# Optimization experiments

Measured on AMD Instinct MI355X. Metric: run time of the kernel, lower is better.

## Reference

```python
import jax, jax.numpy as jnp
import numpy as np

N_NODES = 100000
N_EDGES = 3200000
EMB_DIM = 128


def setup_inputs() -> dict:
    key = jax.random.key(0)
    k_emb, k_w1, k_w2, k_e = jax.random.split(key, 4)
    emb = jax.random.normal(k_emb, (N_NODES, EMB_DIM), dtype=jnp.float32)
    W1 = jax.random.normal(k_w1, (EMB_DIM, 64), dtype=jnp.float32) * (1.0 / np.sqrt(EMB_DIM))
    b1 = jnp.zeros((64,), dtype=jnp.float32)
    W2 = jax.random.normal(k_w2, (64, 32), dtype=jnp.float32) * (1.0 / np.sqrt(64))
    b2 = jnp.zeros((32,), dtype=jnp.float32)
    edge_index = jax.random.randint(k_e, (2, N_EDGES), 0, N_NODES, dtype=jnp.int64)
    return {"embedding": emb, "W1": W1, "b1": b1, "W2": W2, "b2": b2,
            "edge_index": edge_index}


def gcn_conv(x, W, b, src, dst, n):
    # PyG GCNConv defaults: add self-loops, symmetric normalization D^-1/2 (A+I) D^-1/2,
    # linear transform first, then gather-scale-scatter aggregation, then bias.
    xw = x @ W                                                  # [N, out]
    ones = jnp.ones(src.shape, dtype=xw.dtype)
    deg = jax.ops.segment_sum(ones, dst, num_segments=n) + 1.0  # in-degree + self-loop
    dis = jax.lax.rsqrt(deg)                                    # deg >= 1 always
    norm = dis[src] * dis[dst]                                  # [E]
    agg = jax.ops.segment_sum(xw[src] * norm[:, None], dst, num_segments=n)
    agg = agg + (dis * dis)[:, None] * xw                       # self-loop messages
    return agg + b


def reference(embedding, W1, b1, W2, b2, edge_index):
    n = embedding.shape[0]
    src, dst = edge_index[0], edge_index[1]
    # encode
    h = jax.nn.relu(gcn_conv(embedding, W1, b1, src, dst, n))
    z = gcn_conv(h, W2, b2, src, dst, n)                        # [N, 32]
    # decode: per-edge gather-dot-sigmoid
    logits = jnp.sum(z[src] * z[dst], axis=1)                   # [E]
    return jax.nn.sigmoid(logits)
```

## Files before the change

kernel.cpp:

```cpp
#include <hip/hip_runtime.h>
#include <hip/hip_bf16.h>
#include <math.h>

#define NN 100000
#define NE 3200000
#define NPAD 100096
#define NB 196
#define BN 512
#define EPB 8192
#define NBLK 391

__device__ __forceinline__ unsigned short bf16_of(float x) {
    __hip_bfloat16 h = __float2bfloat16(x);
    return *(unsigned short*)&h;
}
__device__ __forceinline__ unsigned pack2(float a, float b) {
    return (unsigned)bf16_of(a) | ((unsigned)bf16_of(b) << 16);
}
__device__ __forceinline__ float lo_f(unsigned u) { return __uint_as_float(u << 16); }
__device__ __forceinline__ float hi_f(unsigned u) { return __uint_as_float(u & 0xffff0000u); }
__device__ __forceinline__ void acc8(float* a, uint4 r) {
    a[0] += lo_f(r.x); a[1] += hi_f(r.x);
    a[2] += lo_f(r.y); a[3] += hi_f(r.y);
    a[4] += lo_f(r.z); a[5] += hi_f(r.z);
    a[6] += lo_f(r.w); a[7] += hi_f(r.w);
}

__global__ __launch_bounds__(256) void hist_kernel(const int* __restrict__ dst,
                                                   int* __restrict__ blkhist) {
    __shared__ int cnt[NB];
    int t = threadIdx.x;
    for (int i = t; i < NB; i += 256) cnt[i] = 0;
    __syncthreads();
    int e0 = blockIdx.x * EPB;
    int e1 = min(e0 + EPB, NE);
    for (int e = e0 + t; e < e1; e += 256) atomicAdd(&cnt[dst[e] >> 9], 1);
    __syncthreads();
    for (int i = t; i < NB; i += 256) blkhist[i * NBLK + blockIdx.x] = cnt[i];
}

__global__ __launch_bounds__(64) void scanA_kernel(int* __restrict__ blkhist,
                                                   int* __restrict__ totals) {
    int j = blockIdx.x, lane = threadIdx.x;
    int base = j * NBLK;
    int carry = 0;
    for (int c = 0; c < NBLK; c += 64) {
        int b = c + lane;
        int v = (b < NBLK) ? blkhist[base + b] : 0;
        int inc = v;
#pragma unroll
        for (int m = 1; m < 64; m <<= 1) {
            int u = __shfl_up(inc, m, 64);
            if (lane >= m) inc += u;
        }
        if (b < NBLK) blkhist[base + b] = carry + inc - v;
        carry += __shfl(inc, 63, 64);
    }
    if (lane == 0) totals[j] = carry;
}

__global__ __launch_bounds__(256) void scanB_kernel(const int* __restrict__ totals,
                                                    int* __restrict__ bucket_base) {
    __shared__ int sm[NB];
    int t = threadIdx.x;
    if (t < NB) sm[t] = totals[t];
    __syncthreads();
    if (t == 0) {
        int r = 0;
        for (int i = 0; i < NB; ++i) { bucket_base[i] = r; r += sm[i]; }
        bucket_base[NB] = r;
    }
}

__global__ __launch_bounds__(256) void scatter_kernel(const int* __restrict__ src,
                                                      const int* __restrict__ dst,
                                                      const int* __restrict__ blkhist,
                                                      const int* __restrict__ bucket_base,
                                                      int* __restrict__ staged) {
    __shared__ int cnt[NB];
    __shared__ int lbase[NB + 1];
    __shared__ int gbase[NB];
    __shared__ int sbuf[EPB];
    int t = threadIdx.x;
    for (int i = t; i < NB; i += 256) cnt[i] = 0;
    __syncthreads();
    int e0 = blockIdx.x * EPB;
    int e1 = min(e0 + EPB, NE);
    int cn = e1 - e0;
    for (int e = e0 + t; e < e1; e += 256) atomicAdd(&cnt[dst[e] >> 9], 1);
    __syncthreads();
    if (t < 64) {
        int v[4]; int s = 0;
#pragma unroll
        for (int k = 0; k < 4; ++k) { int idx = t * 4 + k; v[k] = (idx < NB) ? cnt[idx] : 0; s += v[k]; }
        int inc = s;
#pragma unroll
        for (int m = 1; m < 64; m <<= 1) {
            int u = __shfl_up(inc, m, 64);
            if (t >= m) inc += u;
        }
        int run = inc - s;
#pragma unroll
        for (int k = 0; k < 4; ++k) { int idx = t * 4 + k; if (idx < NB) lbase[idx] = run; run += v[k]; }
        if (t == 63) lbase[NB] = inc;
    }
    __syncthreads();
    for (int i = t; i < NB; i += 256) {
        gbase[i] = bucket_base[i] + blkhist[i * NBLK + blockIdx.x];
        cnt[i] = lbase[i];
    }
    __syncthreads();
    for (int e = e0 + t; e < e1; e += 256) {
        int s = src[e], d = dst[e];
        int r = atomicAdd(&cnt[d >> 9], 1);
        sbuf[r] = (s << 9) | (d & (BN - 1));
    }
    __syncthreads();
    for (int i = t; i < cn; i += 256) {
        int lo = 0, hi = NB - 1;
        while (lo < hi) { int mid = (lo + hi + 1) >> 1; if (lbase[mid] <= i) lo = mid; else hi = mid - 1; }
        staged[gbase[lo] + i - lbase[lo]] = sbuf[i];
    }
}

__global__ __launch_bounds__(256) void fine_kernel(const int* __restrict__ staged,
                                                   const int* __restrict__ bucket_base,
                                                   int* __restrict__ offset,
                                                   float* __restrict__ dis,
                                                   int* __restrict__ csr_src) {
    __shared__ int hist[BN];
    __shared__ int offs[BN];
    __shared__ int cur[BN];
    int t = threadIdx.x, j = blockIdx.x;
    int bb = bucket_base[j], be = bucket_base[j + 1];
    for (int i = t; i < BN; i += 256) hist[i] = 0;
    __syncthreads();
    for (int e = bb + t; e < be; e += 256) atomicAdd(&hist[staged[e] & (BN - 1)], 1);
    __syncthreads();
    if (t < 64) {
        int v[8]; int s = 0;
#pragma unroll
        for (int k = 0; k < 8; ++k) { v[k] = hist[t * 8 + k]; s += v[k]; }
        int inc = s;
#pragma unroll
        for (int m = 1; m < 64; m <<= 1) {
            int u = __shfl_up(inc, m, 64);
            if (t >= m) inc += u;
        }
        int run = inc - s;
#pragma unroll
        for (int k = 0; k < 8; ++k) { offs[t * 8 + k] = run; run += v[k]; }
    }
    __syncthreads();
    for (int l = t; l < BN; l += 256) {
        cur[l] = offs[l];
        int n = j * BN + l;
        if (n < NN) {
            offset[n] = bb + offs[l];
            dis[n] = rsqrtf((float)hist[l] + 1.0f);
        }
    }
    if (j == NB - 1 && t == 0) offset[NN] = NE;
    __syncthreads();
    for (int e = bb + t; e < be; e += 256) {
        int p = staged[e];
        int r = atomicAdd(&cur[p & (BN - 1)], 1);
        csr_src[bb + r] = p >> 9;
    }
}

__global__ __launch_bounds__(256) void mm1_kernel(const float* __restrict__ x,
                                                  const float* __restrict__ W,
                                                  const float* __restrict__ dis,
                                                  unsigned short* __restrict__ y) {
    __shared__ float Ws[128 * 64];
    __shared__ float xs[4][8][132];
    int t = threadIdx.x;
    for (int i = t; i < 128 * 64; i += 256) Ws[i] = W[i];
    int wave = t >> 6, lane = t & 63;
    int nsub = lane >> 3;
    int o8 = (lane & 7) * 8;
    int base = blockIdx.x * 32 + wave * 8;
#pragma unroll
    for (int r = 0; r < 8; ++r) {
        xs[wave][r][lane] = x[(size_t)(base + r) * 128 + lane];
        xs[wave][r][lane + 64] = x[(size_t)(base + r) * 128 + 64 + lane];
    }
    __syncthreads();
    float acc[8] = {0, 0, 0, 0, 0, 0, 0, 0};
#pragma unroll 16
    for (int k = 0; k < 128; ++k) {
        float a = xs[wave][nsub][k];
        const float4 w0 = *(const float4*)&Ws[k * 64 + o8];
        const float4 w1 = *(const float4*)&Ws[k * 64 + o8 + 4];
        acc[0] = fmaf(a, w0.x, acc[0]); acc[1] = fmaf(a, w0.y, acc[1]);
        acc[2] = fmaf(a, w0.z, acc[2]); acc[3] = fmaf(a, w0.w, acc[3]);
        acc[4] = fmaf(a, w1.x, acc[4]); acc[5] = fmaf(a, w1.y, acc[5]);
        acc[6] = fmaf(a, w1.z, acc[6]); acc[7] = fmaf(a, w1.w, acc[7]);
    }
    float sc = dis[base + nsub];
    uint4 o;
    o.x = pack2(acc[0] * sc, acc[1] * sc);
    o.y = pack2(acc[2] * sc, acc[3] * sc);
    o.z = pack2(acc[4] * sc, acc[5] * sc);
    o.w = pack2(acc[6] * sc, acc[7] * sc);
    *(uint4*)&y[(size_t)(base + nsub) * 64 + o8] = o;
}

__global__ __launch_bounds__(256) void mm2_kernel(const unsigned short* __restrict__ h,
                                                  const float* __restrict__ W,
                                                  const float* __restrict__ dis,
                                                  unsigned short* __restrict__ y) {
    __shared__ float Ws[64 * 32];
    __shared__ float hs[4][8][68];
    int t = threadIdx.x;
    for (int i = t; i < 64 * 32; i += 256) Ws[i] = W[i];
    int wave = t >> 6, lane = t & 63;
    int nsub = lane >> 3;
    int o4 = (lane & 7) * 4;
    int base = blockIdx.x * 32 + wave * 8;
    const unsigned* h2 = (const unsigned*)h;
#pragma unroll
    for (int rr = 0; rr < 4; ++rr) {
        int r = rr * 2 + (lane >> 5);
        unsigned u = h2[(size_t)(base + r) * 32 + (lane & 31)];
        hs[wave][r][(lane & 31) * 2] = lo_f(u);
        hs[wave][r][(lane & 31) * 2 + 1] = hi_f(u);
    }
    __syncthreads();
    float4 acc = {0.f, 0.f, 0.f, 0.f};
#pragma unroll 16
    for (int k = 0; k < 64; ++k) {
        float a = hs[wave][nsub][k];
        const float4 w = *(const float4*)&Ws[k * 32 + o4];
        acc.x = fmaf(a, w.x, acc.x);
        acc.y = fmaf(a, w.y, acc.y);
        acc.z = fmaf(a, w.z, acc.z);
        acc.w = fmaf(a, w.w, acc.w);
    }
    float sc = dis[base + nsub];
    ushort4 o;
    o.x = bf16_of(acc.x * sc); o.y = bf16_of(acc.y * sc);
    o.z = bf16_of(acc.z * sc); o.w = bf16_of(acc.w * sc);
    *(ushort4*)&y[(size_t)(base + nsub) * 32 + o4] = o;
}

__global__ __launch_bounds__(256) void agg64_kernel(const uint4* __restrict__ ys4,
                                                    const float* __restrict__ dis,
                                                    const int* __restrict__ offset,
                                                    const int* __restrict__ csr_src,
                                                    const float* __restrict__ b,
                                                    uint4* __restrict__ h4) {
    int tid = blockIdx.x * 256 + threadIdx.x;
    int nd = tid >> 3, c = tid & 7;
    if (nd >= NN) return;
    int start = offset[nd], end = offset[nd + 1];
    float acc[8] = {0, 0, 0, 0, 0, 0, 0, 0};
    acc8(acc, ys4[(size_t)nd * 8 + c]);
    int i = start;
    int n8 = start + ((end - start) & ~7);
    for (; i < n8; i += 8) {
        int s0 = csr_src[i],     s1 = csr_src[i + 1], s2 = csr_src[i + 2], s3 = csr_src[i + 3];
        int s4 = csr_src[i + 4], s5 = csr_src[i + 5], s6 = csr_src[i + 6], s7 = csr_src[i + 7];
        uint4 r0 = ys4[(size_t)s0 * 8 + c];
        uint4 r1 = ys4[(size_t)s1 * 8 + c];
        uint4 r2 = ys4[(size_t)s2 * 8 + c];
        uint4 r3 = ys4[(size_t)s3 * 8 + c];
        uint4 r4 = ys4[(size_t)s4 * 8 + c];
        uint4 r5 = ys4[(size_t)s5 * 8 + c];
        uint4 r6 = ys4[(size_t)s6 * 8 + c];
        uint4 r7 = ys4[(size_t)s7 * 8 + c];
        acc8(acc, r0); acc8(acc, r1); acc8(acc, r2); acc8(acc, r3);
        acc8(acc, r4); acc8(acc, r5); acc8(acc, r6); acc8(acc, r7);
    }
    for (; i < end; ++i) acc8(acc, ys4[(size_t)csr_src[i] * 8 + c]);
    float ds = dis[nd];
    const float4 bv0 = *(const float4*)&b[c * 8];
    const float4 bv1 = *(const float4*)&b[c * 8 + 4];
    uint4 o;
    o.x = pack2(fmaxf(fmaf(ds, acc[0], bv0.x), 0.f), fmaxf(fmaf(ds, acc[1], bv0.y), 0.f));
    o.y = pack2(fmaxf(fmaf(ds, acc[2], bv0.z), 0.f), fmaxf(fmaf(ds, acc[3], bv0.w), 0.f));
    o.z = pack2(fmaxf(fmaf(ds, acc[4], bv1.x), 0.f), fmaxf(fmaf(ds, acc[5], bv1.y), 0.f));
    o.w = pack2(fmaxf(fmaf(ds, acc[6], bv1.z), 0.f), fmaxf(fmaf(ds, acc[7], bv1.w), 0.f));
    h4[(size_t)nd * 8 + c] = o;
}

__global__ __launch_bounds__(256) void agg32_kernel(const uint4* __restrict__ ys4,
                                                    const float* __restrict__ dis,
                                                    const int* __restrict__ offset,
                                                    const int* __restrict__ csr_src,
                                                    const float* __restrict__ b,
                                                    uint4* __restrict__ z4) {
    int tid = blockIdx.x * 256 + threadIdx.x;
    int nd = tid >> 2, c = tid & 3;
    if (nd >= NN) return;
    int start = offset[nd], end = offset[nd + 1];
    float acc[8] = {0, 0, 0, 0, 0, 0, 0, 0};
    acc8(acc, ys4[(size_t)nd * 4 + c]);
    int i = start;
    int n8 = start + ((end - start) & ~7);
    for (; i < n8; i += 8) {
        int s0 = csr_src[i],     s1 = csr_src[i + 1], s2 = csr_src[i + 2], s3 = csr_src[i + 3];
        int s4 = csr_src[i + 4], s5 = csr_src[i + 5], s6 = csr_src[i + 6], s7 = csr_src[i + 7];
        uint4 r0 = ys4[(size_t)s0 * 4 + c];
        uint4 r1 = ys4[(size_t)s1 * 4 + c];
        uint4 r2 = ys4[(size_t)s2 * 4 + c];
        uint4 r3 = ys4[(size_t)s3 * 4 + c];
        uint4 r4 = ys4[(size_t)s4 * 4 + c];
        uint4 r5 = ys4[(size_t)s5 * 4 + c];
        uint4 r6 = ys4[(size_t)s6 * 4 + c];
        uint4 r7 = ys4[(size_t)s7 * 4 + c];
        acc8(acc, r0); acc8(acc, r1); acc8(acc, r2); acc8(acc, r3);
        acc8(acc, r4); acc8(acc, r5); acc8(acc, r6); acc8(acc, r7);
    }
    for (; i < end; ++i) acc8(acc, ys4[(size_t)csr_src[i] * 4 + c]);
    float ds = dis[nd];
    const float4 bv0 = *(const float4*)&b[c * 8];
    const float4 bv1 = *(const float4*)&b[c * 8 + 4];
    uint4 o;
    o.x = pack2(fmaf(ds, acc[0], bv0.x), fmaf(ds, acc[1], bv0.y));
    o.y = pack2(fmaf(ds, acc[2], bv0.z), fmaf(ds, acc[3], bv0.w));
    o.z = pack2(fmaf(ds, acc[4], bv1.x), fmaf(ds, acc[5], bv1.y));
    o.w = pack2(fmaf(ds, acc[6], bv1.z), fmaf(ds, acc[7], bv1.w));
    z4[(size_t)nd * 4 + c] = o;
}

__global__ __launch_bounds__(256) void decode_kernel(const uint4* __restrict__ z4,
                                                     const int* __restrict__ src,
                                                     const int* __restrict__ dst,
                                                     float* __restrict__ out) {
    int tid = blockIdx.x * 256 + threadIdx.x;
    int e = tid >> 2, k = tid & 3;
    if (e >= NE) return;
    int s = src[e], d = dst[e];
    uint4 ra = z4[(size_t)s * 4 + k];
    uint4 rb = z4[(size_t)d * 4 + k];
    float acc;
    acc  = lo_f(ra.x) * lo_f(rb.x) + hi_f(ra.x) * hi_f(rb.x);
    acc += lo_f(ra.y) * lo_f(rb.y) + hi_f(ra.y) * hi_f(rb.y);
    acc += lo_f(ra.z) * lo_f(rb.z) + hi_f(ra.z) * hi_f(rb.z);
    acc += lo_f(ra.w) * lo_f(rb.w) + hi_f(ra.w) * hi_f(rb.w);
#pragma unroll
    for (int m = 2; m >= 1; m >>= 1) acc += __shfl_xor(acc, m, 4);
    if (k == 0) out[e] = 1.0f / (1.0f + expf(-acc));
}

extern "C" void kernel_launch(void* const* d_in, const int* in_sizes, int n_in,
                              void* d_out, int out_size, void* d_ws, size_t ws_size,
                              hipStream_t stream) {
    const float* emb = (const float*)d_in[0];
    const float* W1  = (const float*)d_in[1];
    const float* b1  = (const float*)d_in[2];
    const float* W2  = (const float*)d_in[3];
    const float* b2  = (const float*)d_in[4];
    const int*   ei  = (const int*)d_in[5];
    const int* src = ei;
    const int* dst = ei + NE;
    float* out = (float*)d_out;

    char* w = (char*)d_ws;
    int*   offset      = (int*)w;           w += (size_t)NPAD * 4;
    float* dis         = (float*)w;         w += (size_t)NPAD * 4;
    int*   bucket_base = (int*)w;           w += 1024;
    int*   totals      = (int*)w;           w += 1024;
    int*   blkhist     = (int*)w;           w += 307200;
    int*   csr_src     = (int*)w;           w += (size_t)NE * 4;
    int*   staged      = (int*)w;           w += (size_t)NE * 4;
    unsigned short* ysbuf = (unsigned short*)w; w += (size_t)NN * 64 * 2;
    unsigned short* h  = (unsigned short*)w;
    unsigned short* ys1 = ysbuf;
    unsigned short* ys2 = ysbuf;
    unsigned short* z   = ysbuf + (size_t)NN * 32;

    hist_kernel<<<NBLK, 256, 0, stream>>>(dst, blkhist);
    scanA_kernel<<<NB, 64, 0, stream>>>(blkhist, totals);
    scanB_kernel<<<1, 256, 0, stream>>>(totals, bucket_base);
    scatter_kernel<<<NBLK, 256, 0, stream>>>(src, dst, blkhist, bucket_base, staged);
    fine_kernel<<<NB, 256, 0, stream>>>(staged, bucket_base, offset, dis, csr_src);

    mm1_kernel<<<NN / 32, 256, 0, stream>>>(emb, W1, dis, ys1);
    agg64_kernel<<<(NN * 8) / 256, 256, 0, stream>>>((const uint4*)ys1, dis, offset, csr_src, b1, (uint4*)h);

    mm2_kernel<<<NN / 32, 256, 0, stream>>>(h, W2, dis, ys2);
    agg32_kernel<<<(NN * 4 + 255) / 256, 256, 0, stream>>>((const uint4*)ys2, dis, offset, csr_src, b2, (uint4*)z);

    decode_kernel<<<(NE * 4) / 256, 256, 0, stream>>>((const uint4*)z, src, dst, out);
}
```

Baseline: 398.3 us.

## Use bf16 MFMA for both dense transforms and store bucket ids in scatter

Both node-feature matmuls (128→64 and 64→32) move from scalar FP32 FMA loops to bf16 16x16x32 MFMA instructions. The weights are held transposed in LDS and kept in registers, and each wave processes four 16-row tiles over a 391-block grid. mm1 now converts the FP32 embedding input to bf16 before the matmul, which lowers precision. Separately, the scatter kernel records each edge's bucket id in shared memory, replacing a per-element binary search during write-out at the cost of 8 KB more LDS.

After: 363.3 us. 8.8% less time.

```diff
diff --git a/kernel.cpp b/kernel.cpp
--- a/kernel.cpp
+++ b/kernel.cpp
@@ -9,6 +9,9 @@
 #define BN 512
 #define EPB 8192
 #define NBLK 391
+
+typedef __attribute__((ext_vector_type(8))) short short8;
+typedef __attribute__((ext_vector_type(4))) float floatx4;
 
 __device__ __forceinline__ unsigned short bf16_of(float x) {
     __hip_bfloat16 h = __float2bfloat16(x);
@@ -81,6 +84,7 @@
     __shared__ int lbase[NB + 1];
     __shared__ int gbase[NB];
     __shared__ int sbuf[EPB];
+    __shared__ unsigned char sbkt[EPB];
     int t = threadIdx.x;
     for (int i = t; i < NB; i += 256) cnt[i] = 0;
     __syncthreads();
@@ -112,14 +116,15 @@
     __syncthreads();
     for (int e = e0 + t; e < e1; e += 256) {
         int s = src[e], d = dst[e];
-        int r = atomicAdd(&cnt[d >> 9], 1);
+        int bk = d >> 9;
+        int r = atomicAdd(&cnt[bk], 1);
         sbuf[r] = (s << 9) | (d & (BN - 1));
+        sbkt[r] = (unsigned char)bk;
     }
     __syncthreads();
     for (int i = t; i < cn; i += 256) {
-        int lo = 0, hi = NB - 1;
-        while (lo < hi) { int mid = (lo + hi + 1) >> 1; if (lbase[mid] <= i) lo = mid; else hi = mid - 1; }
-        staged[gbase[lo] + i - lbase[lo]] = sbuf[i];
+        int bk = sbkt[i];
+        staged[gbase[bk] + i - lbase[bk]] = sbuf[i];
     }
 }
 
@@ -173,76 +178,98 @@
                                                   const float* __restrict__ W,
                                                   const float* __restrict__ dis,
                                                   unsigned short* __restrict__ y) {
-    __shared__ float Ws[128 * 64];
-    __shared__ float xs[4][8][132];
+    __shared__ unsigned short Wt[64][136];
     int t = threadIdx.x;
-    for (int i = t; i < 128 * 64; i += 256) Ws[i] = W[i];
+    for (int i = t; i < 128 * 64; i += 256) {
+        int k = i >> 6, n = i & 63;
+        Wt[n][k] = bf16_of(W[i]);
+    }
+    __syncthreads();
     int wave = t >> 6, lane = t & 63;
-    int nsub = lane >> 3;
-    int o8 = (lane & 7) * 8;
-    int base = blockIdx.x * 32 + wave * 8;
-#pragma unroll
-    for (int r = 0; r < 8; ++r) {
-        xs[wave][r][lane] = x[(size_t)(base + r) * 128 + lane];
-        xs[wave][r][lane + 64] = x[(size_t)(base + r) * 128 + 64 + lane];
-    }
-    __syncthreads();
-    float acc[8] = {0, 0, 0, 0, 0, 0, 0, 0};
-#pragma unroll 16
-    for (int k = 0; k < 128; ++k) {
-        float a = xs[wave][nsub][k];
-        const float4 w0 = *(const float4*)&Ws[k * 64 + o8];
-        const float4 w1 = *(const float4*)&Ws[k * 64 + o8 + 4];
-        acc[0] = fmaf(a, w0.x, acc[0]); acc[1] = fmaf(a, w0.y, acc[1]);
-        acc[2] = fmaf(a, w0.z, acc[2]); acc[3] = fmaf(a, w0.w, acc[3]);
-        acc[4] = fmaf(a, w1.x, acc[4]); acc[5] = fmaf(a, w1.y, acc[5]);
-        acc[6] = fmaf(a, w1.z, acc[6]); acc[7] = fmaf(a, w1.w, acc[7]);
-    }
-    float sc = dis[base + nsub];
-    uint4 o;
-    o.x = pack2(acc[0] * sc, acc[1] * sc);
-    o.y = pack2(acc[2] * sc, acc[3] * sc);
-    o.z = pack2(acc[4] * sc, acc[5] * sc);
-    o.w = pack2(acc[6] * sc, acc[7] * sc);
-    *(uint4*)&y[(size_t)(base + nsub) * 64 + o8] = o;
+    int quad = lane >> 4, n16 = lane & 15;
+    short8 bfr[4][4];
+#pragma unroll
+    for (int s = 0; s < 4; ++s)
+#pragma unroll
+        for (int tt = 0; tt < 4; ++tt)
+            bfr[s][tt] = *(const short8*)&Wt[tt * 16 + n16][s * 32 + quad * 8];
+    int tile0 = (blockIdx.x * 4 + wave) * 4;
+#pragma unroll 1
+    for (int it = 0; it < 4; ++it) {
+        int tile = tile0 + it;
+        if (tile >= 6250) break;
+        int m0 = tile * 16;
+        const float* xp = x + (size_t)(m0 + n16) * 128 + quad * 8;
+        floatx4 acc0 = {0,0,0,0}, acc1 = {0,0,0,0}, acc2 = {0,0,0,0}, acc3 = {0,0,0,0};
+#pragma unroll
+        for (int s = 0; s < 4; ++s) {
+            float4 lo = *(const float4*)(xp + s * 32);
+            float4 hi = *(const float4*)(xp + s * 32 + 4);
+            short8 a;
+            a[0] = (short)bf16_of(lo.x); a[1] = (short)bf16_of(lo.y);
+            a[2] = (short)bf16_of(lo.z); a[3] = (short)bf16_of(lo.w);
+            a[4] = (short)bf16_of(hi.x); a[5] = (short)bf16_of(hi.y);
+            a[6] = (short)bf16_of(hi.z); a[7] = (short)bf16_of(hi.w);
+            acc0 = __builtin_amdgcn_mfma_f32_16x16x32_bf16(a, bfr[s][0], acc0, 0, 0, 0);
+            acc1 = __builtin_amdgcn_mfma_f32_16x16x32_bf16(a, bfr[s][1], acc1, 0, 0, 0);
+            acc2 = __builtin_amdgcn_mfma_f32_16x16x32_bf16(a, bfr[s][2], acc2, 0, 0, 0);
+            acc3 = __builtin_amdgcn_mfma_f32_16x16x32_bf16(a, bfr[s][3], acc3, 0, 0, 0);
+        }
+#pragma unroll
+        for (int r = 0; r < 4; ++r) {
+            int ro = m0 + quad * 4 + r;
+            float sc = dis[ro];
+            unsigned short* yp = y + (size_t)ro * 64 + n16;
+            yp[0]  = bf16_of(acc0[r] * sc);
+            yp[16] = bf16_of(acc1[r] * sc);
+            yp[32] = bf16_of(acc2[r] * sc);
+            yp[48] = bf16_of(acc3[r] * sc);
+        }
+    }
 }
 
 __global__ __launch_bounds__(256) void mm2_kernel(const unsigned short* __restrict__ h,
                                                   const float* __restrict__ W,
                                                   const float* __restrict__ dis,
                                                   unsigned short* __restrict__ y) {
-    __shared__ float Ws[64 * 32];
-    __shared__ float hs[4][8][68];
+    __shared__ unsigned short Wt[32][72];
     int t = threadIdx.x;
-    for (int i = t; i < 64 * 32; i += 256) Ws[i] = W[i];
+    for (int i = t; i < 64 * 32; i += 256) {
+        int k = i >> 5, n = i & 31;
+        Wt[n][k] = bf16_of(W[i]);
+    }
+    __syncthreads();
     int wave = t >> 6, lane = t & 63;
-    int nsub = lane >> 3;
-    int o4 = (lane & 7) * 4;
-    int base = blockIdx.x * 32 + wave * 8;
-    const unsigned* h2 = (const unsigned*)h;
-#pragma unroll
-    for (int rr = 0; rr < 4; ++rr) {
-        int r = rr * 2 + (lane >> 5);
-        unsigned u = h2[(size_t)(base + r) * 32 + (lane & 31)];
-        hs[wave][r][(lane & 31) * 2] = lo_f(u);
-        hs[wave][r][(lane & 31) * 2 + 1] = hi_f(u);
-    }
-    __syncthreads();
-    float4 acc = {0.f, 0.f, 0.f, 0.f};
-#pragma unroll 16
-    for (int k = 0; k < 64; ++k) {
-        float a = hs[wave][nsub][k];
-        const float4 w = *(const float4*)&Ws[k * 32 + o4];
-        acc.x = fmaf(a, w.x, acc.x);
-        acc.y = fmaf(a, w.y, acc.y);
-        acc.z = fmaf(a, w.z, acc.z);
-        acc.w = fmaf(a, w.w, acc.w);
-    }
-    float sc = dis[base + nsub];
-    ushort4 o;
-    o.x = bf16_of(acc.x * sc); o.y = bf16_of(acc.y * sc);
-    o.z = bf16_of(acc.z * sc); o.w = bf16_of(acc.w * sc);
-    *(ushort4*)&y[(size_t)(base + nsub) * 32 + o4] = o;
+    int quad = lane >> 4, n16 = lane & 15;
+    short8 bfr[2][2];
+#pragma unroll
+    for (int s = 0; s < 2; ++s)
+#pragma unroll
+        for (int tt = 0; tt < 2; ++tt)
+            bfr[s][tt] = *(const short8*)&Wt[tt * 16 + n16][s * 32 + quad * 8];
+    int tile0 = (blockIdx.x * 4 + wave) * 4;
+#pragma unroll 1
+    for (int it = 0; it < 4; ++it) {
+        int tile = tile0 + it;
+        if (tile >= 6250) break;
+        int m0 = tile * 16;
+        const unsigned short* hp = h + (size_t)(m0 + n16) * 64 + quad * 8;
+        floatx4 acc0 = {0,0,0,0}, acc1 = {0,0,0,0};
+#pragma unroll
+        for (int s = 0; s < 2; ++s) {
+            short8 a = *(const short8*)(hp + s * 32);
+            acc0 = __builtin_amdgcn_mfma_f32_16x16x32_bf16(a, bfr[s][0], acc0, 0, 0, 0);
+            acc1 = __builtin_amdgcn_mfma_f32_16x16x32_bf16(a, bfr[s][1], acc1, 0, 0, 0);
+        }
+#pragma unroll
+        for (int r = 0; r < 4; ++r) {
+            int ro = m0 + quad * 4 + r;
+            float sc = dis[ro];
+            unsigned short* yp = y + (size_t)ro * 32 + n16;
+            yp[0]  = bf16_of(acc0[r] * sc);
+            yp[16] = bf16_of(acc1[r] * sc);
+        }
+    }
 }
 
 __global__ __launch_bounds__(256) void agg64_kernel(const uint4* __restrict__ ys4,
@@ -378,10 +405,10 @@
     scatter_kernel<<<NBLK, 256, 0, stream>>>(src, dst, blkhist, bucket_base, staged);
     fine_kernel<<<NB, 256, 0, stream>>>(staged, bucket_base, offset, dis, csr_src);
 
-    mm1_kernel<<<NN / 32, 256, 0, stream>>>(emb, W1, dis, ys1);
+    mm1_kernel<<<391, 256, 0, stream>>>(emb, W1, dis, ys1);
     agg64_kernel<<<(NN * 8) / 256, 256, 0, stream>>>((const uint4*)ys1, dis, offset, csr_src, b1, (uint4*)h);
 
-    mm2_kernel<<<NN / 32, 256, 0, stream>>>(h, W2, dis, ys2);
+    mm2_kernel<<<391, 256, 0, stream>>>(h, W2, dis, ys2);
     agg32_kernel<<<(NN * 4 + 255) / 256, 256, 0, stream>>>((const uint4*)ys2, dis, offset, csr_src, b2, (uint4*)z);
 
     decode_kernel<<<(NE * 4) / 256, 256, 0, stream>>>((const uint4*)z, src, dst, out);
```
